# Kernel optimization log

Measured on AMD Instinct MI355X. Metric: run time of the kernel, lower is better.

## Reference

```python
import jax, jax.numpy as jnp
import numpy as np

T = 32400   # bs*H*W BEV queries (1*180*180)
S = 16896   # bs*num_cams*h*w image keys (1*6*32*88)
E = 256     # embed_dim
H = 8       # num_heads
D = 32      # head_dim
MAXL = 32   # max interval length (ref_num_f)


def _mlp(x, w1, b1, w2, b2):
    # nn.Sequential(Linear(E,2E), ReLU, Linear(2E,E))
    return jax.nn.relu(x @ w1 + b1) @ w2 + b2


def setup_inputs() -> dict:
    k0 = jax.random.key(0)
    ks = jax.random.split(k0, 8)
    # ragged interval structure: every BEV cell has an interval of length (idx%32)+1
    lengths = (np.arange(T) % MAXL) + 1
    starts = np.concatenate([np.zeros(1, np.int64), np.cumsum(lengths)[:-1]])
    N = int(lengths.sum())  # 534472 frustum points
    ranks_bev = np.repeat(np.arange(T), lengths)          # sorted by BEV cell
    rng = np.random.default_rng(0)
    ranks_feat = rng.integers(0, S, size=N)               # which key/value row each point reads

    def lin(k, fi, fo):
        return jax.random.normal(k, (fi, fo), jnp.float32) * (1.0 / np.sqrt(fi))

    key_feat = jax.random.normal(ks[1], (S, E), jnp.float32)
    return dict(
        query_depth=jax.random.normal(ks[0], (T, E), jnp.float32),
        key=key_feat,
        value=key_feat,  # module asserts torch.equal(key, value)
        q_w1=lin(ks[2], E, 2 * E), q_b1=jnp.zeros((2 * E,), jnp.float32),
        q_w2=lin(ks[3], 2 * E, E), q_b2=jnp.zeros((E,), jnp.float32),
        k_w1=lin(ks[4], E, 2 * E), k_b1=jnp.zeros((2 * E,), jnp.float32),
        k_w2=lin(ks[5], 2 * E, E), k_b2=jnp.zeros((E,), jnp.float32),
        ranks_feat_f=jnp.asarray(ranks_feat, jnp.int32),
        ranks_bev_f=jnp.asarray(ranks_bev, jnp.int32),
        interval_starts_f=jnp.asarray(starts, jnp.int32),
        interval_lengths_f=jnp.asarray(lengths, jnp.int32),
        ref_num=MAXL,
    )


def reference(query_depth, key, value,
              q_w1, q_b1, q_w2, q_b2,
              k_w1, k_b1, k_w2, k_b2,
              ranks_feat_f, ranks_bev_f,
              interval_starts_f, interval_lengths_f, ref_num):
    scaling = 1.0 / jnp.sqrt(jnp.float32(D))
    q = (_mlp(query_depth, q_w1, q_b1, q_w2, q_b2) * scaling).reshape(T, H, D)
    k = _mlp(key, k_w1, k_b1, k_w2, k_b2).reshape(S, H, D)
    v = value.reshape(S, H, D)

    N = ranks_bev_f.shape[0]
    pt = jnp.arange(N, dtype=jnp.int32)
    # interval id of each point (intervals are contiguous, sorted by start)
    iid = jnp.searchsorted(interval_starts_f, pt, side='right') - 1
    ranks_ref = pt - interval_starts_f[iid]  # within-interval slot, in [0, ref_num)

    # per-point raw attention logit: q[bev] . k[feat] per head  -> [N, H]
    w = jnp.einsum('nhd,nhd->nh', q[ranks_bev_f], k[ranks_feat_f])

    # scatter into ragged weight tensor [T, H, ref_num]; padding masked to -1e9
    attn = jnp.full((T, H, ref_num), -1e9, jnp.float32)
    attn = attn.at[ranks_bev_f, :, ranks_ref].set(w)
    attn = jax.nn.softmax(attn, axis=-1)

    # gather normalized weights back per point and scatter-combine values
    wp = attn[ranks_bev_f, :, ranks_ref]          # [N, H]
    vp = v[ranks_feat_f]                          # [N, H, D]
    out = jnp.zeros((T, H, D), jnp.float32).at[ranks_bev_f].add(wp[:, :, None] * vp)
    return out.reshape(T, E)
```

## Files before the change

### kernel.cpp

```cpp
#include <hip/hip_runtime.h>
#include <hip/hip_bf16.h>
#include <cstdint>
#include <cstddef>

constexpr int T_Q   = 32400;
constexpr int T_PAD = 32512;
constexpr int S_K   = 16896;
constexpr int E_DIM = 256;
constexpr int HID   = 512;

typedef __bf16 bf16x8 __attribute__((ext_vector_type(8)));
typedef float  f32x4  __attribute__((ext_vector_type(4)));
typedef unsigned short ushort8v __attribute__((ext_vector_type(8)));

__device__ __forceinline__ void async16(const __hip_bfloat16* gp, __hip_bfloat16* lp) {
    __builtin_amdgcn_global_load_lds(
        (const __attribute__((address_space(1))) void*)(gp),
        (__attribute__((address_space(3))) void*)(lp), 16, 0, 0);
}

__device__ __forceinline__ float b2f(unsigned short u) {
    return __uint_as_float(((unsigned)u) << 16);
}

constexpr int NB_Q = (T_PAD * E_DIM / 4) / 256;
constexpr int NB_K = (S_K * E_DIM / 4) / 256;
constexpr int NB_PREP = NB_Q + NB_K + NB_K + 128;

__global__ __launch_bounds__(256) void prep(
    const float* __restrict__ q_in, const float* __restrict__ key_in,
    const float* __restrict__ val_in,
    const float* __restrict__ s0, const float* __restrict__ s1,
    const float* __restrict__ s2, const float* __restrict__ s3,
    __hip_bfloat16* __restrict__ qA, __hip_bfloat16* __restrict__ kA,
    __hip_bfloat16* __restrict__ kvB,
    __hip_bfloat16* __restrict__ d0, __hip_bfloat16* __restrict__ d1,
    __hip_bfloat16* __restrict__ d2, __hip_bfloat16* __restrict__ d3) {
    __shared__ float tb[64][65];
    const int b = blockIdx.x;
    const int tid = threadIdx.x;

    if (b < NB_Q + 2 * NB_K) {
        const float* src;
        int bl, valid, isv = 0;
        if (b < NB_Q) { src = q_in; bl = b; valid = T_Q * E_DIM; }
        else if (b < NB_Q + NB_K) { src = key_in; bl = b - NB_Q; valid = S_K * E_DIM; }
        else { src = val_in; bl = b - NB_Q - NB_K; valid = S_K * E_DIM; isv = 1; }
        int i = (bl * 256 + tid) * 4;
        float4 f = make_float4(0.f, 0.f, 0.f, 0.f);
        if (i < valid) f = *(const float4*)(src + i);
        union { ushort4 u4; __hip_bfloat16 bb[4]; } cv;
        cv.bb[0] = __float2bfloat16(f.x);
        cv.bb[1] = __float2bfloat16(f.y);
        cv.bb[2] = __float2bfloat16(f.z);
        cv.bb[3] = __float2bfloat16(f.w);
        if (isv) {
            int r = i >> 8, c = i & 255;
            *(ushort4*)(kvB + (size_t)r * 512 + 256 + c) = cv.u4;
        } else {
            __hip_bfloat16* dst = (b < NB_Q) ? qA : kA;
            *(ushort4*)(dst + i) = cv.u4;
        }
        return;
    }

    int tloc = b - (NB_Q + 2 * NB_K);
    int m = tloc >> 5;
    int tt = tloc & 31;
    const float* S = m == 0 ? s0 : m == 1 ? s1 : m == 2 ? s2 : s3;
    __hip_bfloat16* D = m == 0 ? d0 : m == 1 ? d1 : m == 2 ? d2 : d3;
    int Kd, Nd, kt, nt;
    if ((m & 1) == 0) { Kd = 256; Nd = 512; kt = tt & 3; nt = tt >> 2; }
    else              { Kd = 512; Nd = 256; kt = tt & 7; nt = tt >> 3; }
    int tx = tid & 63, ty = tid >> 6;
#pragma unroll
    for (int p = 0; p < 16; ++p) {
        int row = ty * 16 + p;
        tb[row][tx] = S[(size_t)(kt * 64 + row) * Nd + nt * 64 + tx];
    }
    __syncthreads();
#pragma unroll
    for (int p = 0; p < 16; ++p) {
        int row = ty * 16 + p;
        D[(size_t)(nt * 64 + row) * Kd + kt * 64 + tx] = __float2bfloat16(tb[tx][row]);
    }
}

constexpr int BM = 128, BN = 128, BK = 32;

__global__ __launch_bounds__(256) void gemm_bf16(
    const __hip_bfloat16* __restrict__ A,
    const __hip_bfloat16* __restrict__ BT,
    const float* __restrict__ bias,
    __hip_bfloat16* __restrict__ C,
    int K, int N, int ldc, int relu, float scale) {
    __shared__ __hip_bfloat16 As[BM * BK];
    __shared__ __hip_bfloat16 Bs[BN * BK];

    const int ntiles = N >> 7;
    const int tm = blockIdx.x / ntiles;
    const int tn = blockIdx.x - tm * ntiles;
    const size_t m0 = (size_t)tm * BM;
    const int n0 = tn * BN;

    const int tid = threadIdx.x;
    const int w = tid >> 6, l = tid & 63;
    const int lm = l & 15, lq = l >> 4;
    const int wm = (w >> 1) << 6, wn = (w & 1) << 6;

    const int srow = l >> 2;
    const int scol = (((l & 3) ^ (srow & 3)) << 3);

    f32x4 acc[4][4] = {};

    for (int k0 = 0; k0 < K; k0 += BK) {
#pragma unroll
        for (int c = 0; c < 2; ++c) {
            int r = c * 64 + w * 16 + srow;
            async16(A  + (m0 + r) * K + k0 + scol, As + (c * 64 + w * 16) * BK);
            async16(BT + (size_t)(n0 + r) * K + k0 + scol, Bs + (c * 64 + w * 16) * BK);
        }
        __syncthreads();

        const int rsw = ((lq ^ (lm & 3)) << 3);
        bf16x8 af[4], bfr[4];
#pragma unroll
        for (int mi = 0; mi < 4; ++mi)
            af[mi] = *(const bf16x8*)(As + (wm + mi * 16 + lm) * BK + rsw);
#pragma unroll
        for (int ni = 0; ni < 4; ++ni)
            bfr[ni] = *(const bf16x8*)(Bs + (wn + ni * 16 + lm) * BK + rsw);
#pragma unroll
        for (int mi = 0; mi < 4; ++mi)
#pragma unroll
            for (int ni = 0; ni < 4; ++ni)
                acc[mi][ni] = __builtin_amdgcn_mfma_f32_16x16x32_bf16(
                    af[mi], bfr[ni], acc[mi][ni], 0, 0, 0);
        __syncthreads();
    }

#pragma unroll
    for (int ni = 0; ni < 4; ++ni) {
        int col = n0 + wn + ni * 16 + lm;
        float bv = bias[col];
#pragma unroll
        for (int mi = 0; mi < 4; ++mi) {
            size_t rowb = m0 + wm + mi * 16 + lq * 4;
#pragma unroll
            for (int r = 0; r < 4; ++r) {
                float vv = acc[mi][ni][r] + bv;
                if (relu) vv = fmaxf(vv, 0.f);
                C[(rowb + r) * ldc + col] = __float2bfloat16(vv * scale);
            }
        }
    }
}

#define APREF(DK, DV, C)                                                    \
    {                                                                       \
        int pidx = ((C) << 1) + half;                                       \
        int f = __builtin_amdgcn_ds_bpermute(pidx << 2, myf);               \
        const __hip_bfloat16* bp = kv + (size_t)f * 512 + sub * 8;          \
        DK = *(const ushort8v*)bp;                                          \
        DV = *(const ushort8v*)(bp + 256);                                  \
    }

#define APROC(KB, VB, C)                                                    \
    {                                                                       \
        float wv = 0.f;                                                     \
        _Pragma("unroll") for (int i = 0; i < 8; ++i)                       \
            wv = fmaf(qf[i], b2f(KB[i]), wv);                               \
        wv += __shfl_xor(wv, 1);                                            \
        wv += __shfl_xor(wv, 2);                                            \
        float wo = __shfl_xor(wv, 32);                                      \
        int pm = ((C) << 1) + half;                                         \
        int po = ((C) << 1) + 1 - half;                                     \
        if (pm >= L) wv = -1e30f;                                           \
        if (po >= L) wo = -1e30f;                                           \
        float mn = fmaxf(m, fmaxf(wv, wo));                                 \
        float al = __expf(m - mn); m = mn;                                  \
        float p = __expf(wv - mn);                                          \
        s = fmaf(s, al, p);                                                 \
        _Pragma("unroll") for (int i = 0; i < 8; ++i)                       \
            a[i] = fmaf(p, b2f(VB[i]), a[i] * al);                          \
    }

__global__ __launch_bounds__(256) void attn_kernel(
    const __hip_bfloat16* __restrict__ q,
    const __hip_bfloat16* __restrict__ kv,
    const int* __restrict__ rf,
    const int* __restrict__ starts,
    const int* __restrict__ lens,
    float* __restrict__ out) {
    int t = blockIdx.x * 4 + (threadIdx.x >> 6);
    if (t >= T_Q) return;
    int l = threadIdx.x & 63;
    int half = l >> 5, sub = l & 31;
    int su = __builtin_amdgcn_readfirstlane(starts[t]);
    int L  = __builtin_amdgcn_readfirstlane(lens[t]);

    int li = l < L - 1 ? l : L - 1;
    int myf = rf[su + li];

    ushort8v qu = *(const ushort8v*)(q + (size_t)t * 256 + sub * 8);
    float qf[8];
#pragma unroll
    for (int i = 0; i < 8; ++i) qf[i] = b2f(qu[i]);

    float m = -INFINITY, s = 0.f;
    float a[8] = {0.f, 0.f, 0.f, 0.f, 0.f, 0.f, 0.f, 0.f};

    ushort8v k0v = {}, v0v = {}, k1v = {}, v1v = {}, k2v = {}, v2v = {};

    int nC = (L + 1) >> 1;
    APREF(k0v, v0v, 0);
    if (nC > 1) APREF(k1v, v1v, 1);
    for (int c = 0; c < nC; ++c) {
        if (c + 2 < nC) APREF(k2v, v2v, c + 2);
        APROC(k0v, v0v, c);
        k0v = k1v; v0v = v1v;
        k1v = k2v; v1v = v2v;
    }

    s += __shfl_xor(s, 32);
#pragma unroll
    for (int i = 0; i < 8; ++i) a[i] += __shfl_xor(a[i], 32);
    float inv = 1.f / s;
    float4 o;
    o.x = (half ? a[4] : a[0]) * inv;
    o.y = (half ? a[5] : a[1]) * inv;
    o.z = (half ? a[6] : a[2]) * inv;
    o.w = (half ? a[7] : a[3]) * inv;
    *(float4*)(out + (size_t)t * 256 + sub * 8 + half * 4) = o;
}

extern "C" void kernel_launch(void* const* d_in, const int* in_sizes, int n_in,
                              void* d_out, int out_size, void* d_ws, size_t ws_size,
                              hipStream_t stream) {
    const float* q_in   = (const float*)d_in[0];
    const float* key_in = (const float*)d_in[1];
    const float* val_in = (const float*)d_in[2];
    const float* q_w1   = (const float*)d_in[3];
    const float* q_b1   = (const float*)d_in[4];
    const float* q_w2   = (const float*)d_in[5];
    const float* q_b2   = (const float*)d_in[6];
    const float* k_w1   = (const float*)d_in[7];
    const float* k_b1   = (const float*)d_in[8];
    const float* k_w2   = (const float*)d_in[9];
    const float* k_b2   = (const float*)d_in[10];
    const int* ranks_feat = (const int*)d_in[11];
    const int* starts     = (const int*)d_in[13];
    const int* lens       = (const int*)d_in[14];
    float* out = (float*)d_out;

    char* ws = (char*)d_ws;
    size_t off = 0;
    auto alloc = [&](size_t bytes) {
        char* p = ws + off;
        off += (bytes + 255) & ~(size_t)255;
        return p;
    };
    __hip_bfloat16* qA   = (__hip_bfloat16*)alloc((size_t)T_PAD * E_DIM * 2);
    __hip_bfloat16* hidQ = (__hip_bfloat16*)alloc((size_t)T_PAD * HID * 2);
    __hip_bfloat16* qMl  = (__hip_bfloat16*)alloc((size_t)T_PAD * E_DIM * 2);
    __hip_bfloat16* kA   = (__hip_bfloat16*)alloc((size_t)S_K * E_DIM * 2);
    __hip_bfloat16* hidK = (__hip_bfloat16*)alloc((size_t)S_K * HID * 2);
    __hip_bfloat16* kvB  = (__hip_bfloat16*)alloc((size_t)S_K * 512 * 2);
    __hip_bfloat16* w1qT = (__hip_bfloat16*)alloc((size_t)HID * E_DIM * 2);
    __hip_bfloat16* w2qT = (__hip_bfloat16*)alloc((size_t)E_DIM * HID * 2);
    __hip_bfloat16* w1kT = (__hip_bfloat16*)alloc((size_t)HID * E_DIM * 2);
    __hip_bfloat16* w2kT = (__hip_bfloat16*)alloc((size_t)E_DIM * HID * 2);
    (void)ws_size; (void)n_in; (void)out_size; (void)in_sizes;

    prep<<<NB_PREP, 256, 0, stream>>>(q_in, key_in, val_in,
                                      q_w1, q_w2, k_w1, k_w2,
                                      qA, kA, kvB, w1qT, w2qT, w1kT, w2kT);

    const float qscale = 0.17677669529663687f;
    gemm_bf16<<<(T_PAD / 128) * (HID / 128), 256, 0, stream>>>(qA, w1qT, q_b1, hidQ, E_DIM, HID, HID, 1, 1.0f);
    gemm_bf16<<<(T_PAD / 128) * (E_DIM / 128), 256, 0, stream>>>(hidQ, w2qT, q_b2, qMl, HID, E_DIM, E_DIM, 0, qscale);
    gemm_bf16<<<(S_K / 128) * (HID / 128), 256, 0, stream>>>(kA, w1kT, k_b1, hidK, E_DIM, HID, HID, 1, 1.0f);
    gemm_bf16<<<(S_K / 128) * (E_DIM / 128), 256, 0, stream>>>(hidK, w2kT, k_b2, kvB, HID, E_DIM, 512, 0, 1.0f);

    attn_kernel<<<T_Q / 4, 256, 0, stream>>>(qMl, kvB, ranks_feat, starts, lens, out);
}
```

Measured before the change: 313.1 us.

## Merge Q/K MLP GEMMs into dual launches and batch attention gathers

The four MLP GEMM launches become two, each covering both the query and key tiles, so the launch count drops and each grid is larger with fewer idle CUs in the tail. The attention kernel stops using an online-softmax loop with a rolling prefetch of two chunks. It now issues all key and value gathers for up to 16 chunks at once, then runs a two-pass softmax. This exposes more memory-level parallelism for the random gathers, at the cost of much higher register pressure (32 ushort8 vectors plus offsets), which may reduce occupancy.

```diff
diff --git a/kernel.cpp b/kernel.cpp
--- a/kernel.cpp
+++ b/kernel.cpp
@@ -88,19 +88,27 @@
 
 constexpr int BM = 128, BN = 128, BK = 32;
 
-__global__ __launch_bounds__(256) void gemm_bf16(
-    const __hip_bfloat16* __restrict__ A,
-    const __hip_bfloat16* __restrict__ BT,
-    const float* __restrict__ bias,
-    __hip_bfloat16* __restrict__ C,
-    int K, int N, int ldc, int relu, float scale) {
+__global__ __launch_bounds__(256) void gemm_dual(
+    const __hip_bfloat16* __restrict__ Aq, const __hip_bfloat16* __restrict__ Ak,
+    const __hip_bfloat16* __restrict__ BTq, const __hip_bfloat16* __restrict__ BTk,
+    const float* __restrict__ biasq, const float* __restrict__ biask,
+    __hip_bfloat16* __restrict__ Cq, __hip_bfloat16* __restrict__ Ck,
+    int K, int N, int ldcq, int ldck, int relu,
+    float scaleq, float scalek, int qtiles) {
     __shared__ __hip_bfloat16 As[BM * BK];
     __shared__ __hip_bfloat16 Bs[BN * BK];
 
     const int ntiles = N >> 7;
     const int tm = blockIdx.x / ntiles;
     const int tn = blockIdx.x - tm * ntiles;
-    const size_t m0 = (size_t)tm * BM;
+    const bool isq = tm < qtiles;
+    const __hip_bfloat16* A  = isq ? Aq : Ak;
+    const __hip_bfloat16* BT = isq ? BTq : BTk;
+    const float* bias = isq ? biasq : biask;
+    __hip_bfloat16* C = isq ? Cq : Ck;
+    const int ldc = isq ? ldcq : ldck;
+    const float scale = isq ? scaleq : scalek;
+    const size_t m0 = (size_t)(isq ? tm : tm - qtiles) * BM;
     const int n0 = tn * BN;
 
     const int tid = threadIdx.x;
@@ -155,35 +163,6 @@
         }
     }
 }
-
-#define APREF(DK, DV, C)                                                    \
-    {                                                                       \
-        int pidx = ((C) << 1) + half;                                       \
-        int f = __builtin_amdgcn_ds_bpermute(pidx << 2, myf);               \
-        const __hip_bfloat16* bp = kv + (size_t)f * 512 + sub * 8;          \
-        DK = *(const ushort8v*)bp;                                          \
-        DV = *(const ushort8v*)(bp + 256);                                  \
-    }
-
-#define APROC(KB, VB, C)                                                    \
-    {                                                                       \
-        float wv = 0.f;                                                     \
-        _Pragma("unroll") for (int i = 0; i < 8; ++i)                       \
-            wv = fmaf(qf[i], b2f(KB[i]), wv);                               \
-        wv += __shfl_xor(wv, 1);                                            \
-        wv += __shfl_xor(wv, 2);                                            \
-        float wo = __shfl_xor(wv, 32);                                      \
-        int pm = ((C) << 1) + half;                                         \
-        int po = ((C) << 1) + 1 - half;                                     \
-        if (pm >= L) wv = -1e30f;                                           \
-        if (po >= L) wo = -1e30f;                                           \
-        float mn = fmaxf(m, fmaxf(wv, wo));                                 \
-        float al = __expf(m - mn); m = mn;                                  \
-        float p = __expf(wv - mn);                                          \
-        s = fmaf(s, al, p);                                                 \
-        _Pragma("unroll") for (int i = 0; i < 8; ++i)                       \
-            a[i] = fmaf(p, b2f(VB[i]), a[i] * al);                          \
-    }
 
 __global__ __launch_bounds__(256) void attn_kernel(
     const __hip_bfloat16* __restrict__ q,
@@ -198,33 +177,65 @@
     int half = l >> 5, sub = l & 31;
     int su = __builtin_amdgcn_readfirstlane(starts[t]);
     int L  = __builtin_amdgcn_readfirstlane(lens[t]);
+    int nC = (L + 1) >> 1;
 
     int li = l < L - 1 ? l : L - 1;
     int myf = rf[su + li];
 
+    const char* base = (const char*)kv;
+    unsigned voff[16];
+#pragma unroll
+    for (int c = 0; c < 16; ++c) {
+        int f = __shfl(myf, 2 * c + half);
+        voff[c] = ((unsigned)f << 10) + (unsigned)(sub << 4);
+    }
+
     ushort8v qu = *(const ushort8v*)(q + (size_t)t * 256 + sub * 8);
     float qf[8];
 #pragma unroll
     for (int i = 0; i < 8; ++i) qf[i] = b2f(qu[i]);
 
-    float m = -INFINITY, s = 0.f;
+    ushort8v kb[16], vb[16];
+#pragma unroll
+    for (int c = 0; c < 16; ++c)
+        if (c < nC) kb[c] = *(const ushort8v*)(base + voff[c]);
+
+    float w[16];
+#pragma unroll
+    for (int c = 0; c < 16; ++c) w[c] = -1e30f;
+#pragma unroll
+    for (int c = 0; c < 16; ++c) {
+        if (c < nC) {
+            vb[c] = *(const ushort8v*)(base + voff[c] + 512);
+            float wv = 0.f;
+#pragma unroll
+            for (int i = 0; i < 8; ++i) wv = fmaf(qf[i], b2f(kb[c][i]), wv);
+            wv += __shfl_xor(wv, 1);
+            wv += __shfl_xor(wv, 2);
+            w[c] = (2 * c + half < L) ? wv : -1e30f;
+        }
+    }
+
+    float mx = -1e30f;
+#pragma unroll
+    for (int c = 0; c < 16; ++c) mx = fmaxf(mx, w[c]);
+    mx = fmaxf(mx, __shfl_xor(mx, 32));
+    float s = 0.f;
+#pragma unroll
+    for (int c = 0; c < 16; ++c) { w[c] = __expf(w[c] - mx); s += w[c]; }
+    s += __shfl_xor(s, 32);
+
     float a[8] = {0.f, 0.f, 0.f, 0.f, 0.f, 0.f, 0.f, 0.f};
-
-    ushort8v k0v = {}, v0v = {}, k1v = {}, v1v = {}, k2v = {}, v2v = {};
-
-    int nC = (L + 1) >> 1;
-    APREF(k0v, v0v, 0);
-    if (nC > 1) APREF(k1v, v1v, 1);
-    for (int c = 0; c < nC; ++c) {
-        if (c + 2 < nC) APREF(k2v, v2v, c + 2);
-        APROC(k0v, v0v, c);
-        k0v = k1v; v0v = v1v;
-        k1v = k2v; v1v = v2v;
-    }
-
-    s += __shfl_xor(s, 32);
+#pragma unroll
+    for (int c = 0; c < 16; ++c) {
+        if (c < nC) {
+#pragma unroll
+            for (int i = 0; i < 8; ++i) a[i] = fmaf(w[c], b2f(vb[c][i]), a[i]);
+        }
+    }
 #pragma unroll
     for (int i = 0; i < 8; ++i) a[i] += __shfl_xor(a[i], 32);
+
     float inv = 1.f / s;
     float4 o;
     o.x = (half ? a[4] : a[0]) * inv;
@@ -277,10 +288,15 @@
                                       qA, kA, kvB, w1qT, w2qT, w1kT, w2kT);
 
     const float qscale = 0.17677669529663687f;
-    gemm_bf16<<<(T_PAD / 128) * (HID / 128), 256, 0, stream>>>(qA, w1qT, q_b1, hidQ, E_DIM, HID, HID, 1, 1.0f);
-    gemm_bf16<<<(T_PAD / 128) * (E_DIM / 128), 256, 0, stream>>>(hidQ, w2qT, q_b2, qMl, HID, E_DIM, E_DIM, 0, qscale);
-    gemm_bf16<<<(S_K / 128) * (HID / 128), 256, 0, stream>>>(kA, w1kT, k_b1, hidK, E_DIM, HID, HID, 1, 1.0f);
-    gemm_bf16<<<(S_K / 128) * (E_DIM / 128), 256, 0, stream>>>(hidK, w2kT, k_b2, kvB, HID, E_DIM, 512, 0, 1.0f);
+    const int QT = T_PAD / 128;
+    const int KT = S_K / 128;
+
+    gemm_dual<<<(QT + KT) * (HID / 128), 256, 0, stream>>>(
+        qA, kA, w1qT, w1kT, q_b1, k_b1, hidQ, hidK,
+        E_DIM, HID, HID, HID, 1, 1.0f, 1.0f, QT);
+    gemm_dual<<<(QT + KT) * (E_DIM / 128), 256, 0, stream>>>(
+        hidQ, hidK, w2qT, w2kT, q_b2, k_b2, qMl, kvB,
+        HID, E_DIM, E_DIM, 512, 0, qscale, 1.0f, QT);
 
     attn_kernel<<<T_Q / 4, 256, 0, stream>>>(qMl, kvB, ranks_feat, starts, lens, out);
 }
```

Measured after the change: 319.2 us. No clear change (+1.9%).
